# Optimization experiments

Measured on AMD Instinct MI355X. Metric: run time of the kernel, lower is better.

## Reference

```python
import jax, jax.numpy as jnp
import numpy as np

N = 25000        # nodes
E = 400000       # edges (avg degree 16)
F_IN = 256       # input node feature dim
C = 32           # tensor-product channels (linear_1 output)
A = 9            # spherical-harmonic dim (lmax=2)
WNUM = C * A     # per-edge TP weight numel (_head_weight_numel)
B = 8            # radial basis size (edge embedding)
H = 64           # edge MLP hidden width
S = 4            # species (node_attrs one-hot width)
F_OUT = 256      # output node feature dim
AVG_NEIGH = 16.0


def setup_inputs() -> dict:
    key = jax.random.key(0)
    ks = jax.random.split(key, 11)
    sc = lambda fan: np.float32(1.0 / np.sqrt(fan))
    return {
        "x": jax.random.normal(ks[0], (N, F_IN), jnp.float32),
        "node_attrs": jax.random.uniform(ks[1], (N, S), jnp.float32),
        "edge_embedding": jax.random.uniform(ks[2], (E, B), jnp.float32),
        "edge_attr": jax.random.normal(ks[3], (E, A), jnp.float32),
        "edge_index": jax.random.randint(ks[4], (2, E), 0, N, jnp.int32),
        "W1": jax.random.normal(ks[5], (F_IN, C), jnp.float32) * sc(F_IN),
        "Wm1": jax.random.normal(ks[6], (B, H), jnp.float32) * sc(B),
        "Wm2": jax.random.normal(ks[7], (H, H), jnp.float32) * sc(H),
        "Wm3": jax.random.normal(ks[8], (H, WNUM), jnp.float32) * sc(H),
        "W2": jax.random.normal(ks[9], (WNUM, F_OUT), jnp.float32) * sc(WNUM),
        "Wsc": jax.random.normal(ks[10], (F_IN, S, F_OUT), jnp.float32) * sc(F_IN * S),
    }


def reference(x, node_attrs, edge_embedding, edge_attr, edge_index,
              W1, Wm1, Wm2, Wm3, W2, Wsc):
    # self-connection: FullyConnectedTensorProduct(x, node_attrs) -> [N, F_OUT]
    sc_out = jnp.einsum('nf,ns,fso->no', x, node_attrs, Wsc)

    # linear_1 + avg-neighbor normalization -> [N, C]
    h = (x @ W1) * (1.0 / jnp.sqrt(jnp.asarray(AVG_NEIGH, x.dtype)))

    # edge MLP on radial embedding -> per-edge TP weights [E, C, A]
    w = jax.nn.silu(edge_embedding @ Wm1)
    w = jax.nn.silu(w @ Wm2)
    w = (w @ Wm3).reshape(E, C, A)

    edge_dst = edge_index[0]
    edge_src = edge_index[1]

    # gather-TP-scatter: msg[e,c,a] = w[e,c,a] * h[src[e],c] * sh[e,a]
    msg = w * h[edge_src][:, :, None] * edge_attr[:, None, :]   # [E, C, A]
    agg = jax.ops.segment_sum(msg.reshape(E, WNUM), edge_dst,
                              num_segments=N)                    # [N, C*A]

    # linear_2 + activation + self-connection
    out = jax.nn.silu(agg @ W2) + sc_out                         # [N, F_OUT]
    return out
```

## Files before the change

### kernel.cpp

```cpp
#include <hip/hip_runtime.h>

#define NN   25000
#define EE   400000
#define FIN  256
#define CC   32
#define AA   9
#define WN   288
#define BB   8
#define HH   64
#define SS   4
#define FOUT 256
#define EPB  64

typedef float f32x4 __attribute__((ext_vector_type(4)));
typedef short short8 __attribute__((ext_vector_type(8)));

__device__ __forceinline__ float silu_f(float v){ return v / (1.0f + __expf(-v)); }

__device__ __forceinline__ unsigned short f2bf(float f){
  unsigned int u = __builtin_bit_cast(unsigned int, f);
  u += 0x7FFFu + ((u >> 16) & 1u);
  return (unsigned short)(u >> 16);
}

__global__ __launch_bounds__(256) void k_h(const float* __restrict__ x,
                                           const float* __restrict__ W1,
                                           float* __restrict__ h){
  int gid = blockIdx.x * 256 + threadIdx.x;
  int n = gid >> 5, c = gid & 31;
  const float* xr = x + (size_t)n * FIN;
  float acc = 0.f;
  #pragma unroll 8
  for (int f = 0; f < FIN; ++f) acc = fmaf(xr[f], W1[f * CC + c], acc);
  h[gid] = acc * 0.25f;
}

__global__ __launch_bounds__(256) void k_cvt(const float* __restrict__ Wm2,
                                             const float* __restrict__ Wm3,
                                             unsigned short* __restrict__ wm2t,
                                             unsigned short* __restrict__ wm3t){
  int i = blockIdx.x * 256 + threadIdx.x;
  if (i < HH * HH){
    int n = i >> 6, k = i & 63;
    wm2t[n * 64 + k] = f2bf(Wm2[k * HH + n]);
  }
  if (i < WN * HH){
    int n = i >> 6, k = i & 63;
    wm3t[n * 64 + k] = f2bf(Wm3[k * WN + n]);
  }
}

__global__ __launch_bounds__(256) void k_cvtsc(const float* __restrict__ Wsc,
                                               unsigned short* __restrict__ wscb){
  __shared__ float tile[32][33];
  const int k0 = blockIdx.x * 32;
  const int n0 = blockIdx.y * 32;
  const int t = threadIdx.x;
  #pragma unroll
  for (int p = 0; p < 4; ++p){
    int idx = t + p * 256;
    int r = idx >> 5, c = idx & 31;
    tile[r][c] = Wsc[(size_t)(k0 + r) * 256 + n0 + c];
  }
  __syncthreads();
  #pragma unroll
  for (int p = 0; p < 4; ++p){
    int idx = t + p * 256;
    int r = idx >> 5, c = idx & 31;
    wscb[(size_t)(n0 + r) * 1024 + k0 + c] = f2bf(tile[c][r]);
  }
}

__global__ __launch_bounds__(256) void k_hist(const int* __restrict__ eidx,
                                              int* __restrict__ cnt){
  int e = blockIdx.x * 256 + threadIdx.x;
  if (e < EE) atomicAdd(&cnt[eidx[e]], 1);
}

__global__ __launch_bounds__(1024) void k_scan(const int* __restrict__ cnt,
                                               int* __restrict__ cur){
  __shared__ int part[1024];
  const int t = threadIdx.x;
  const int base = t * 25;
  int s = 0;
  for (int i = 0; i < 25; ++i){
    int idx = base + i;
    s += (idx < NN) ? cnt[idx] : 0;
  }
  part[t] = s;
  __syncthreads();
  for (int off = 1; off < 1024; off <<= 1){
    int v = (t >= off) ? part[t - off] : 0;
    __syncthreads();
    part[t] += v;
    __syncthreads();
  }
  int run = part[t] - s;
  for (int i = 0; i < 25; ++i){
    int idx = base + i;
    if (idx < NN){
      cur[idx] = run;
      run += cnt[idx];
    }
  }
}

__global__ __launch_bounds__(256) void k_scatter(const int* __restrict__ eidx,
                                                 int* __restrict__ cur,
                                                 int* __restrict__ perm){
  int e = blockIdx.x * 256 + threadIdx.x;
  if (e < EE){
    int d = eidx[e];
    int p = atomicAdd(&cur[d], 1);
    perm[p] = e;
  }
}

__global__ __launch_bounds__(256) void k_sc(const float* __restrict__ x,
                                            const float* __restrict__ na,
                                            const unsigned short* __restrict__ wscb,
                                            float* __restrict__ out){
  __shared__ __align__(16) unsigned short As[64][72];
  __shared__ __align__(16) unsigned short Bs[256][72];
  const int tid = threadIdx.x;
  const int m0 = blockIdx.x * 64;
  const int sm = tid >> 2;
  const int sq = tid & 3;
  float4 nav = {0.f, 0.f, 0.f, 0.f};
  if (m0 + sm < NN) nav = *(const float4*)&na[(size_t)(m0 + sm) * SS];
  const float nf[4] = {nav.x, nav.y, nav.z, nav.w};
  const int lane = tid & 63, wv = tid >> 6;
  const int row = lane & 15, kg = lane >> 4;
  const f32x4 zf = {0.f, 0.f, 0.f, 0.f};
  f32x4 acc[16];
  #pragma unroll
  for (int i = 0; i < 16; ++i) acc[i] = zf;

  for (int kc = 0; kc < FIN * SS; kc += 64){
    __syncthreads();
    {
      float4 xv = {0.f, 0.f, 0.f, 0.f};
      int fc4 = (kc >> 2) + sq * 4;
      if (m0 + sm < NN) xv = *(const float4*)&x[(size_t)(m0 + sm) * FIN + fc4];
      float xf[4] = {xv.x, xv.y, xv.z, xv.w};
      unsigned short tmp[16];
      #pragma unroll
      for (int f = 0; f < 4; ++f)
        #pragma unroll
        for (int s = 0; s < 4; ++s) tmp[f * 4 + s] = f2bf(xf[f] * nf[s]);
      *(short8*)&As[sm][sq * 16]     = *(short8*)&tmp[0];
      *(short8*)&As[sm][sq * 16 + 8] = *(short8*)&tmp[8];
    }
    #pragma unroll
    for (int r = 0; r < 4; ++r){
      int ch = tid + r * 256;
      int n = ch >> 2, c4 = ch & 3;
      const unsigned short* src = wscb + (size_t)n * 1024 + kc + c4 * 16;
      *(short8*)&Bs[n][c4 * 16]     = *(const short8*)src;
      *(short8*)&Bs[n][c4 * 16 + 8] = *(const short8*)(src + 8);
    }
    __syncthreads();
    #pragma unroll
    for (int ks = 0; ks < 2; ++ks){
      short8 af = *(const short8*)&As[wv * 16 + row][ks * 32 + kg * 8];
      #pragma unroll
      for (int nt = 0; nt < 16; ++nt){
        short8 bfr = *(const short8*)&Bs[nt * 16 + row][ks * 32 + kg * 8];
        acc[nt] = __builtin_amdgcn_mfma_f32_16x16x32_bf16(af, bfr, acc[nt], 0, 0, 0);
      }
    }
  }
  #pragma unroll
  for (int nt = 0; nt < 16; ++nt){
    #pragma unroll
    for (int r = 0; r < 4; ++r){
      int m = m0 + wv * 16 + kg * 4 + r;
      if (m < NN) out[(size_t)m * FOUT + nt * 16 + row] = acc[nt][r];
    }
  }
}

__global__ __launch_bounds__(256) void k_edge(const float* __restrict__ eemb,
                                              const float* __restrict__ sh,
                                              const int* __restrict__ eidx,
                                              const int* __restrict__ perm,
                                              const float* __restrict__ h,
                                              const float* __restrict__ Wm1,
                                              const unsigned short* __restrict__ wm2t,
                                              const unsigned short* __restrict__ wm3t,
                                              float* __restrict__ agg){
  __shared__ float ee_s[EPB][8];
  __shared__ float sh_s[EPB][12];
  __shared__ float hs_s[EPB][32];
  __shared__ int   dst_s[EPB];
  __shared__ int   src_s[EPB];
  __shared__ int   pe_s[EPB];
  __shared__ __align__(16) unsigned short t1b[EPB][72];
  __shared__ __align__(16) unsigned short t2b[EPB][72];
  const int tid = threadIdx.x;
  const int e0 = blockIdx.x * EPB;

  if (tid < EPB){
    int pe = perm[e0 + tid];
    pe_s[tid]  = pe;
    dst_s[tid] = eidx[pe];
    src_s[tid] = eidx[EE + pe];
  }
  __syncthreads();
  { int i = tid;        int e = i >> 3, b = i & 7; ee_s[e][b] = eemb[(size_t)pe_s[e] * BB + b]; }
  { int i = tid + 256;  int e = i >> 3, b = i & 7; ee_s[e][b] = eemb[(size_t)pe_s[e] * BB + b]; }
  for (int i = tid; i < EPB * AA; i += 256){
    int e = i / 9, a = i - e * 9;
    sh_s[e][a] = sh[(size_t)pe_s[e] * AA + a];
  }
  #pragma unroll
  for (int r = 0; r < 8; ++r){
    int i = tid + r * 256;
    int e = i >> 5, c = i & 31;
    hs_s[e][c] = h[(size_t)src_s[e] * CC + c];
  }
  __syncthreads();

  {
    const int j2 = tid & 31;
    const int eg = tid >> 5;
    float w0[8], w1[8];
    #pragma unroll
    for (int b = 0; b < 8; ++b){
      w0[b] = Wm1[b * HH + 2 * j2];
      w1[b] = Wm1[b * HH + 2 * j2 + 1];
    }
    #pragma unroll
    for (int e8 = 0; e8 < 8; ++e8){
      int e = eg * 8 + e8;
      float a0 = 0.f, a1 = 0.f;
      #pragma unroll
      for (int b = 0; b < 8; ++b){
        float ev = ee_s[e][b];
        a0 = fmaf(ev, w0[b], a0);
        a1 = fmaf(ev, w1[b], a1);
      }
      a0 = silu_f(a0); a1 = silu_f(a1);
      unsigned int pk = (unsigned int)f2bf(a0) | ((unsigned int)f2bf(a1) << 16);
      *(unsigned int*)&t1b[e][j2 * 2] = pk;
    }
  }

  const int lane = tid & 63;
  const int wv   = tid >> 6;
  const int row  = lane & 15;
  const int kg   = lane >> 4;
  const f32x4 zf = {0.f, 0.f, 0.f, 0.f};

  {
    short8 a2k0 = *(const short8*)&t1b[wv * 16 + row][kg * 8];
    short8 a2k1 = *(const short8*)&t1b[wv * 16 + row][kg * 8 + 32];
    #pragma unroll
    for (int nt = 0; nt < 4; ++nt){
      const unsigned short* bp = wm2t + (size_t)((nt * 16 + row) * 64 + kg * 8);
      short8 b0 = *(const short8*)bp;
      short8 b1 = *(const short8*)(bp + 32);
      f32x4 acc = __builtin_amdgcn_mfma_f32_16x16x32_bf16(a2k0, b0, zf, 0, 0, 0);
      acc = __builtin_amdgcn_mfma_f32_16x16x32_bf16(a2k1, b1, acc, 0, 0, 0);
      #pragma unroll
      for (int r = 0; r < 4; ++r){
        int e = wv * 16 + kg * 4 + r;
        t2b[e][nt * 16 + row] = f2bf(silu_f(acc[r]));
      }
    }
  }

  {
    short8 a3k0 = *(const short8*)&t2b[wv * 16 + row][kg * 8];
    short8 a3k1 = *(const short8*)&t2b[wv * 16 + row][kg * 8 + 32];
    const int ebase = wv * 16 + kg * 4;
    for (int nt = 0; nt < 18; ++nt){
      const unsigned short* bp = wm3t + (size_t)((nt * 16 + row) * 64 + kg * 8);
      short8 b0 = *(const short8*)bp;
      short8 b1 = *(const short8*)(bp + 32);
      f32x4 acc = __builtin_amdgcn_mfma_f32_16x16x32_bf16(a3k0, b0, zf, 0, 0, 0);
      acc = __builtin_amdgcn_mfma_f32_16x16x32_bf16(a3k1, b1, acc, 0, 0, 0);
      int j = nt * 16 + row;
      int c = j / 9, a_ = j - c * 9;
      float vals[4];
      #pragma unroll
      for (int r = 0; r < 4; ++r){
        int e = ebase + r;
        vals[r] = acc[r] * hs_s[e][c] * sh_s[e][a_];
      }
      #pragma unroll
      for (int r = 0; r < 4; ++r){
        int e = ebase + r;
        int d = dst_s[e];
        bool last = (r == 3) || (dst_s[e + 1] != d);
        if (!last){
          vals[r + 1] += vals[r];
        } else {
          atomicAdd(&agg[(size_t)d * WN + j], vals[r]);
        }
      }
    }
  }
}

__global__ __launch_bounds__(256) void k_out(const float* __restrict__ agg,
                                             const float* __restrict__ W2,
                                             float* __restrict__ out){
  __shared__ float As[32][68];
  __shared__ float Bs[32][64];
  const int row0 = blockIdx.x * 64;
  const int col0 = blockIdx.y * 64;
  const int tid = threadIdx.x;
  const int tm = tid >> 4, tn = tid & 15;
  float acc[4][4] = {};
  for (int kc = 0; kc < WN; kc += 32){
    #pragma unroll
    for (int t = 0; t < 8; ++t){
      int idx = tid + t * 256;
      int m = idx >> 5, kk = idx & 31;
      int n = row0 + m;
      float v = 0.f;
      if (n < NN) v = agg[(size_t)n * WN + kc + kk];
      As[kk][m] = v;
    }
    #pragma unroll
    for (int t = 0; t < 8; ++t){
      int idx = tid + t * 256;
      int o = idx & 63, kk = idx >> 6;
      Bs[kk][o] = W2[(size_t)(kc + kk) * FOUT + col0 + o];
    }
    __syncthreads();
    #pragma unroll
    for (int kk = 0; kk < 32; ++kk){
      float4 av = *(const float4*)&As[kk][tm * 4];
      float4 bv = *(const float4*)&Bs[kk][tn * 4];
      float a[4] = {av.x, av.y, av.z, av.w};
      float b[4] = {bv.x, bv.y, bv.z, bv.w};
      #pragma unroll
      for (int i = 0; i < 4; ++i)
        #pragma unroll
        for (int j = 0; j < 4; ++j)
          acc[i][j] = fmaf(a[i], b[j], acc[i][j]);
    }
    __syncthreads();
  }
  #pragma unroll
  for (int i = 0; i < 4; ++i){
    int n = row0 + tm * 4 + i;
    if (n < NN){
      float4 sc = *(const float4*)&out[(size_t)n * FOUT + col0 + tn * 4];
      float4 v;
      v.x = silu_f(acc[i][0]) + sc.x;
      v.y = silu_f(acc[i][1]) + sc.y;
      v.z = silu_f(acc[i][2]) + sc.z;
      v.w = silu_f(acc[i][3]) + sc.w;
      *(float4*)&out[(size_t)n * FOUT + col0 + tn * 4] = v;
    }
  }
}

extern "C" void kernel_launch(void* const* d_in, const int* in_sizes, int n_in,
                              void* d_out, int out_size, void* d_ws, size_t ws_size,
                              hipStream_t stream){
  const float* x    = (const float*)d_in[0];
  const float* na   = (const float*)d_in[1];
  const float* eemb = (const float*)d_in[2];
  const float* shp  = (const float*)d_in[3];
  const int*   eidx = (const int*)d_in[4];
  const float* W1   = (const float*)d_in[5];
  const float* Wm1  = (const float*)d_in[6];
  const float* Wm2  = (const float*)d_in[7];
  const float* Wm3  = (const float*)d_in[8];
  const float* W2   = (const float*)d_in[9];
  const float* Wsc  = (const float*)d_in[10];
  float* out  = (float*)d_out;
  float* agg  = (float*)d_ws;
  float* hbuf = agg + (size_t)NN * WN;
  int*   cnt  = (int*)(hbuf + (size_t)NN * CC);
  int*   cur  = cnt + NN;
  int*   perm = cur + NN;
  unsigned short* wm2t = (unsigned short*)(perm + EE);
  unsigned short* wm3t = wm2t + HH * HH;
  unsigned short* wscb = wm3t + WN * HH;

  hipMemsetAsync(agg, 0, (size_t)NN * WN * sizeof(float), stream);
  hipMemsetAsync(cnt, 0, (size_t)NN * sizeof(int), stream);
  k_cvt    <<<dim3((WN * HH + 255) / 256), dim3(256), 0, stream>>>(Wm2, Wm3, wm2t, wm3t);
  k_cvtsc  <<<dim3(32, 8), dim3(256), 0, stream>>>(Wsc, wscb);
  k_hist   <<<dim3((EE + 255) / 256), dim3(256),  0, stream>>>(eidx, cnt);
  k_scan   <<<dim3(1),                dim3(1024), 0, stream>>>(cnt, cur);
  k_scatter<<<dim3((EE + 255) / 256), dim3(256),  0, stream>>>(eidx, cur, perm);
  k_h  <<<dim3(NN * CC / 256), dim3(256), 0, stream>>>(x, W1, hbuf);
  k_sc <<<dim3((NN + 63) / 64), dim3(256), 0, stream>>>(x, na, wscb, out);
  k_edge<<<dim3(EE / EPB), dim3(256), 0, stream>>>(eemb, shp, eidx, perm, hbuf, Wm1, wm2t, wm3t, agg);
  k_out<<<dim3((NN + 63) / 64, FOUT / 64), dim3(256), 0, stream>>>(agg, W2, out);
}
```

Baseline: 647.0 us.

## Pre-permute edge data in scatter, use MFMA for first MLP layer, shrink edge blocks

The scatter kernel now writes edge embeddings (as bf16), spherical harmonics, src and dst directly into dst-sorted order. The edge kernel therefore reads contiguous data instead of gathering through a permutation array. The first MLP layer moves from scalar FMAs to a zero-padded bf16 MFMA. The edge kernel also uses 32-edge, 128-thread blocks with an XCD-aware block swizzle, hoists the channel/harmonic index arithmetic, and prefetches the Wm3 fragments. This trades extra scatter-time writes and workspace, plus bf16 rounding of the embeddings, for cheaper edge-kernel memory access.

```diff
diff --git a/kernel.cpp b/kernel.cpp
--- a/kernel.cpp
+++ b/kernel.cpp
@@ -10,7 +10,7 @@
 #define HH   64
 #define SS   4
 #define FOUT 256
-#define EPB  64
+#define EPB  32
 
 typedef float f32x4 __attribute__((ext_vector_type(4)));
 typedef short short8 __attribute__((ext_vector_type(8)));
@@ -35,11 +35,17 @@
   h[gid] = acc * 0.25f;
 }
 
-__global__ __launch_bounds__(256) void k_cvt(const float* __restrict__ Wm2,
+__global__ __launch_bounds__(256) void k_cvt(const float* __restrict__ Wm1,
+                                             const float* __restrict__ Wm2,
                                              const float* __restrict__ Wm3,
+                                             unsigned short* __restrict__ wm1t,
                                              unsigned short* __restrict__ wm2t,
                                              unsigned short* __restrict__ wm3t){
   int i = blockIdx.x * 256 + threadIdx.x;
+  if (i < HH * 32){
+    int n = i >> 5, k = i & 31;
+    wm1t[i] = (k < BB) ? f2bf(Wm1[k * HH + n]) : (unsigned short)0;
+  }
   if (i < HH * HH){
     int n = i >> 6, k = i & 63;
     wm2t[n * 64 + k] = f2bf(Wm2[k * HH + n]);
@@ -106,13 +112,26 @@
 }
 
 __global__ __launch_bounds__(256) void k_scatter(const int* __restrict__ eidx,
+                                                 const float* __restrict__ eemb,
+                                                 const float* __restrict__ sh,
                                                  int* __restrict__ cur,
-                                                 int* __restrict__ perm){
+                                                 unsigned short* __restrict__ ee_p,
+                                                 float* __restrict__ sh_p,
+                                                 int* __restrict__ src_p,
+                                                 int* __restrict__ dst_p){
   int e = blockIdx.x * 256 + threadIdx.x;
   if (e < EE){
     int d = eidx[e];
     int p = atomicAdd(&cur[d], 1);
-    perm[p] = e;
+    dst_p[p] = d;
+    src_p[p] = eidx[EE + e];
+    float4 v0 = *(const float4*)&eemb[(size_t)e * BB];
+    float4 v1 = *(const float4*)&eemb[(size_t)e * BB + 4];
+    unsigned short t[8] = {f2bf(v0.x), f2bf(v0.y), f2bf(v0.z), f2bf(v0.w),
+                           f2bf(v1.x), f2bf(v1.y), f2bf(v1.z), f2bf(v1.w)};
+    *(short8*)&ee_p[(size_t)p * BB] = *(short8*)t;
+    #pragma unroll
+    for (int a = 0; a < AA; ++a) sh_p[(size_t)p * AA + a] = sh[(size_t)e * AA + a];
   }
 }
 
@@ -180,77 +199,58 @@
   }
 }
 
-__global__ __launch_bounds__(256) void k_edge(const float* __restrict__ eemb,
-                                              const float* __restrict__ sh,
-                                              const int* __restrict__ eidx,
-                                              const int* __restrict__ perm,
+__global__ __launch_bounds__(128) void k_edge(const unsigned short* __restrict__ ee_p,
+                                              const float* __restrict__ sh_p,
+                                              const int* __restrict__ src_p,
+                                              const int* __restrict__ dst_p,
                                               const float* __restrict__ h,
-                                              const float* __restrict__ Wm1,
+                                              const unsigned short* __restrict__ wm1t,
                                               const unsigned short* __restrict__ wm2t,
                                               const unsigned short* __restrict__ wm3t,
                                               float* __restrict__ agg){
-  __shared__ float ee_s[EPB][8];
-  __shared__ float sh_s[EPB][12];
-  __shared__ float hs_s[EPB][32];
-  __shared__ int   dst_s[EPB];
-  __shared__ int   src_s[EPB];
-  __shared__ int   pe_s[EPB];
+  __shared__ float sh_s[EPB][13];
+  __shared__ float hs_s[EPB][36];
   __shared__ __align__(16) unsigned short t1b[EPB][72];
   __shared__ __align__(16) unsigned short t2b[EPB][72];
   const int tid = threadIdx.x;
-  const int e0 = blockIdx.x * EPB;
-
-  if (tid < EPB){
-    int pe = perm[e0 + tid];
-    pe_s[tid]  = pe;
-    dst_s[tid] = eidx[pe];
-    src_s[tid] = eidx[EE + pe];
+
+  const int nwg = EE / EPB;
+  const int q = nwg >> 3, rr = nwg & 7;
+  int bid = blockIdx.x;
+  int xcd = bid & 7, li = bid >> 3;
+  int swz = (xcd < rr ? xcd * (q + 1) : rr * (q + 1) + (xcd - rr) * q) + li;
+  const int e0 = swz * EPB;
+
+  {
+    int e = tid >> 2, c0 = (tid & 3) * 8;
+    const float* hr = h + (size_t)src_p[e0 + e] * CC + c0;
+    *(float4*)&hs_s[e][c0]     = *(const float4*)hr;
+    *(float4*)&hs_s[e][c0 + 4] = *(const float4*)(hr + 4);
+  }
+  for (int i = tid; i < EPB * AA; i += 128){
+    int e = i / 9, a = i - e * 9;
+    sh_s[e][a] = sh_p[(size_t)e0 * AA + i];
   }
   __syncthreads();
-  { int i = tid;        int e = i >> 3, b = i & 7; ee_s[e][b] = eemb[(size_t)pe_s[e] * BB + b]; }
-  { int i = tid + 256;  int e = i >> 3, b = i & 7; ee_s[e][b] = eemb[(size_t)pe_s[e] * BB + b]; }
-  for (int i = tid; i < EPB * AA; i += 256){
-    int e = i / 9, a = i - e * 9;
-    sh_s[e][a] = sh[(size_t)pe_s[e] * AA + a];
-  }
-  #pragma unroll
-  for (int r = 0; r < 8; ++r){
-    int i = tid + r * 256;
-    int e = i >> 5, c = i & 31;
-    hs_s[e][c] = h[(size_t)src_s[e] * CC + c];
-  }
-  __syncthreads();
-
-  {
-    const int j2 = tid & 31;
-    const int eg = tid >> 5;
-    float w0[8], w1[8];
-    #pragma unroll
-    for (int b = 0; b < 8; ++b){
-      w0[b] = Wm1[b * HH + 2 * j2];
-      w1[b] = Wm1[b * HH + 2 * j2 + 1];
-    }
-    #pragma unroll
-    for (int e8 = 0; e8 < 8; ++e8){
-      int e = eg * 8 + e8;
-      float a0 = 0.f, a1 = 0.f;
-      #pragma unroll
-      for (int b = 0; b < 8; ++b){
-        float ev = ee_s[e][b];
-        a0 = fmaf(ev, w0[b], a0);
-        a1 = fmaf(ev, w1[b], a1);
-      }
-      a0 = silu_f(a0); a1 = silu_f(a1);
-      unsigned int pk = (unsigned int)f2bf(a0) | ((unsigned int)f2bf(a1) << 16);
-      *(unsigned int*)&t1b[e][j2 * 2] = pk;
-    }
-  }
 
   const int lane = tid & 63;
   const int wv   = tid >> 6;
   const int row  = lane & 15;
   const int kg   = lane >> 4;
   const f32x4 zf = {0.f, 0.f, 0.f, 0.f};
+
+  {
+    short8 a1 = {0, 0, 0, 0, 0, 0, 0, 0};
+    if (kg == 0) a1 = *(const short8*)&ee_p[(size_t)(e0 + wv * 16 + row) * BB];
+    #pragma unroll
+    for (int nt = 0; nt < 4; ++nt){
+      short8 b = *(const short8*)&wm1t[(nt * 16 + row) * 32 + kg * 8];
+      f32x4 acc = __builtin_amdgcn_mfma_f32_16x16x32_bf16(a1, b, zf, 0, 0, 0);
+      #pragma unroll
+      for (int r = 0; r < 4; ++r)
+        t1b[wv * 16 + kg * 4 + r][nt * 16 + row] = f2bf(silu_f(acc[r]));
+    }
+  }
 
   {
     short8 a2k0 = *(const short8*)&t1b[wv * 16 + row][kg * 8];
@@ -263,10 +263,8 @@
       f32x4 acc = __builtin_amdgcn_mfma_f32_16x16x32_bf16(a2k0, b0, zf, 0, 0, 0);
       acc = __builtin_amdgcn_mfma_f32_16x16x32_bf16(a2k1, b1, acc, 0, 0, 0);
       #pragma unroll
-      for (int r = 0; r < 4; ++r){
-        int e = wv * 16 + kg * 4 + r;
-        t2b[e][nt * 16 + row] = f2bf(silu_f(acc[r]));
-      }
+      for (int r = 0; r < 4; ++r)
+        t2b[wv * 16 + kg * 4 + r][nt * 16 + row] = f2bf(silu_f(acc[r]));
     }
   }
 
@@ -274,31 +272,38 @@
     short8 a3k0 = *(const short8*)&t2b[wv * 16 + row][kg * 8];
     short8 a3k1 = *(const short8*)&t2b[wv * 16 + row][kg * 8 + 32];
     const int ebase = wv * 16 + kg * 4;
+    int4 dv = *(const int4*)&dst_p[e0 + ebase];
+    const int d[4] = {dv.x, dv.y, dv.z, dv.w};
+    int c  = (row >= 9) ? 1 : 0;
+    int a_ = row - 9 * c;
+    const unsigned short* bp = wm3t + (size_t)(row * 64 + kg * 8);
+    short8 b0n = *(const short8*)bp;
+    short8 b1n = *(const short8*)(bp + 32);
     for (int nt = 0; nt < 18; ++nt){
-      const unsigned short* bp = wm3t + (size_t)((nt * 16 + row) * 64 + kg * 8);
-      short8 b0 = *(const short8*)bp;
-      short8 b1 = *(const short8*)(bp + 32);
+      short8 b0 = b0n, b1 = b1n;
+      if (nt < 17){
+        const unsigned short* bp2 = wm3t + (size_t)(((nt + 1) * 16 + row) * 64 + kg * 8);
+        b0n = *(const short8*)bp2;
+        b1n = *(const short8*)(bp2 + 32);
+      }
       f32x4 acc = __builtin_amdgcn_mfma_f32_16x16x32_bf16(a3k0, b0, zf, 0, 0, 0);
       acc = __builtin_amdgcn_mfma_f32_16x16x32_bf16(a3k1, b1, acc, 0, 0, 0);
       int j = nt * 16 + row;
-      int c = j / 9, a_ = j - c * 9;
       float vals[4];
       #pragma unroll
+      for (int r = 0; r < 4; ++r)
+        vals[r] = acc[r] * hs_s[ebase + r][c] * sh_s[ebase + r][a_];
+      #pragma unroll
       for (int r = 0; r < 4; ++r){
-        int e = ebase + r;
-        vals[r] = acc[r] * hs_s[e][c] * sh_s[e][a_];
-      }
-      #pragma unroll
-      for (int r = 0; r < 4; ++r){
-        int e = ebase + r;
-        int d = dst_s[e];
-        bool last = (r == 3) || (dst_s[e + 1] != d);
+        bool last = (r == 3) || (d[r + 1] != d[r]);
         if (!last){
           vals[r + 1] += vals[r];
         } else {
-          atomicAdd(&agg[(size_t)d * WN + j], vals[r]);
+          atomicAdd(&agg[(size_t)d[r] * WN + j], vals[r]);
         }
       }
+      a_ += 7; c += 1;
+      if (a_ >= 9){ a_ -= 9; c += 1; }
     }
   }
 }
@@ -374,24 +379,31 @@
   const float* W2   = (const float*)d_in[9];
   const float* Wsc  = (const float*)d_in[10];
   float* out  = (float*)d_out;
+
   float* agg  = (float*)d_ws;
   float* hbuf = agg + (size_t)NN * WN;
-  int*   cnt  = (int*)(hbuf + (size_t)NN * CC);
+  float* sh_p = hbuf + (size_t)NN * CC;
+  int*   cnt  = (int*)(sh_p + (size_t)EE * AA);
   int*   cur  = cnt + NN;
-  int*   perm = cur + NN;
-  unsigned short* wm2t = (unsigned short*)(perm + EE);
+  int*   src_p = cur + NN;
+  int*   dst_p = src_p + EE;
+  unsigned short* ee_p = (unsigned short*)(dst_p + EE);
+  unsigned short* wm1t = ee_p + (size_t)EE * BB;
+  unsigned short* wm2t = wm1t + HH * 32;
   unsigned short* wm3t = wm2t + HH * HH;
   unsigned short* wscb = wm3t + WN * HH;
 
   hipMemsetAsync(agg, 0, (size_t)NN * WN * sizeof(float), stream);
   hipMemsetAsync(cnt, 0, (size_t)NN * sizeof(int), stream);
-  k_cvt    <<<dim3((WN * HH + 255) / 256), dim3(256), 0, stream>>>(Wm2, Wm3, wm2t, wm3t);
+  k_cvt    <<<dim3((WN * HH + 255) / 256), dim3(256), 0, stream>>>(Wm1, Wm2, Wm3, wm1t, wm2t, wm3t);
   k_cvtsc  <<<dim3(32, 8), dim3(256), 0, stream>>>(Wsc, wscb);
   k_hist   <<<dim3((EE + 255) / 256), dim3(256),  0, stream>>>(eidx, cnt);
   k_scan   <<<dim3(1),                dim3(1024), 0, stream>>>(cnt, cur);
-  k_scatter<<<dim3((EE + 255) / 256), dim3(256),  0, stream>>>(eidx, cur, perm);
+  k_scatter<<<dim3((EE + 255) / 256), dim3(256),  0, stream>>>(eidx, eemb, shp, cur,
+                                                               ee_p, sh_p, src_p, dst_p);
   k_h  <<<dim3(NN * CC / 256), dim3(256), 0, stream>>>(x, W1, hbuf);
   k_sc <<<dim3((NN + 63) / 64), dim3(256), 0, stream>>>(x, na, wscb, out);
-  k_edge<<<dim3(EE / EPB), dim3(256), 0, stream>>>(eemb, shp, eidx, perm, hbuf, Wm1, wm2t, wm3t, agg);
+  k_edge<<<dim3(EE / EPB), dim3(128), 0, stream>>>(ee_p, sh_p, src_p, dst_p, hbuf,
+                                                   wm1t, wm2t, wm3t, agg);
   k_out<<<dim3((NN + 63) / 64, FOUT / 64), dim3(256), 0, stream>>>(agg, W2, out);
 }
```

After: 657.9 us. No clear change (+1.7%).
